# Kernel tuning notes

Measured on AMD Instinct MI355X. Metric: run time of the kernel, lower is better.

The kernel has to match this reference:

```python
import jax, jax.numpy as jnp
import numpy as np

N = 50000   # nodes
D = 128     # hidden dim
E_NS = 250000  # non-self-loop edges
B = 4096    # sessions
NEG_SLOPE = 0.01  # F.leaky_relu default


def setup_inputs() -> dict:
    key = jax.random.key(0)
    ks = jax.random.split(key, 8)
    x = jax.random.normal(ks[0], (N, D), jnp.float32)
    src = jax.random.randint(ks[1], (E_NS,), 0, N)
    off = jax.random.randint(ks[2], (E_NS,), 1, N)
    dst = (src + off) % N  # guarantees src != dst
    loops = jnp.arange(N)
    edge_index = jnp.stack([jnp.concatenate([src, loops]),
                            jnp.concatenate([dst, loops])])  # [2, E_NS+N]
    batch = jnp.sort(jax.random.randint(ks[3], (N,), 0, B))
    local_sess_avg = jax.random.normal(ks[4], (B, D), jnp.float32)
    stdv = 1.0 / np.sqrt(D)
    W_alpha = jax.random.uniform(ks[5], (1, D), jnp.float32, -stdv, stdv)
    W_forward = jax.random.uniform(ks[6], (1, D), jnp.float32, -stdv, stdv)
    W_backward = jax.random.uniform(ks[7], (1, D), jnp.float32, -stdv, stdv)
    mt_sess_masks = jnp.ones((N,), jnp.int32)
    return {"x": x, "W_alpha": W_alpha, "W_forward": W_forward,
            "W_backward": W_backward, "local_sess_avg": local_sess_avg,
            "edge_index": edge_index, "batch": batch,
            "mt_sess_masks": mt_sess_masks, "n_nonself": E_NS}


def reference(x, W_alpha, W_forward, W_backward, local_sess_avg,
              edge_index, batch, mt_sess_masks, n_nonself):
    n = x.shape[0]
    src, dst = edge_index[0], edge_index[1]
    # non-self-loop edges occupy the first n_nonself columns (static int)
    src_ns, dst_ns = src[:n_nonself], dst[:n_nonself]
    # expanded edges = original edges + reversed non-self-loop edges
    exp_src = jnp.concatenate([src, dst_ns])  # [Et]
    exp_dst = jnp.concatenate([dst, src_ns])  # [Et]

    lrelu = lambda v: jax.nn.leaky_relu(v, NEG_SLOPE)

    exp_xi = x[exp_dst]                     # [Et, D]
    exp_xj = x[exp_src]                     # [Et, D]
    alpha_query = local_sess_avg[batch[exp_dst]]  # [Et, D]
    alpha = lrelu((exp_xi * alpha_query) @ W_alpha.T)        # [Et, 1]
    beta = lrelu((x[dst] * x[src]) @ W_forward.T)            # [E, 1]
    rbeta = lrelu((x[dst_ns] * x[src_ns]) @ W_backward.T)    # [E_ns, 1]
    logits = (jnp.concatenate([beta, rbeta], axis=0) + alpha)[:, 0]  # [Et]

    # segment softmax over target nodes (every node has a self-loop)
    seg_max = jax.lax.stop_gradient(
        jax.ops.segment_max(logits, exp_dst, num_segments=n))
    ex = jnp.exp(logits - seg_max[exp_dst])
    denom = jax.ops.segment_sum(ex, exp_dst, num_segments=n)
    aij = ex / denom[exp_dst]

    # scatter-add weighted neighbor features
    aggr = jax.ops.segment_sum(aij[:, None] * exp_xj, exp_dst, num_segments=n)

    # update: masked nodes take aggregate, others keep x; residual add
    new_x = jnp.where((mt_sess_masks == 1)[:, None], aggr, x)
    return new_x + x
```

## Files before the change

kernel.cpp:

```cpp
#include <hip/hip_runtime.h>

#define NEG_SLOPE 0.01f
#define STRIDE 48

__device__ __forceinline__ float lrelu(float v) { return v > 0.f ? v : NEG_SLOPE * v; }

__device__ __forceinline__ float dot4(float4 a, float4 b) {
    return a.x * b.x + a.y * b.y + a.z * b.z + a.w * b.w;
}

__device__ __forceinline__ void placeEdge(int s, int d, unsigned flag,
                                          int* __restrict__ cursor, int* __restrict__ slots) {
    int pos = atomicAdd(&cursor[d], 1);
    if (pos < STRIDE) slots[d * STRIDE + pos] = (int)((unsigned)s | flag);
}

__global__ void fill_kernel(const int* __restrict__ EI0, const int* __restrict__ EI1,
                            int* __restrict__ cursor, int* __restrict__ slots,
                            int E_total, int E_NS) {
    int t = blockIdx.x * blockDim.x + threadIdx.x;
    int n1v = E_total >> 2, n0v = E_NS >> 2;
    if (t < n1v) {
        int4 s = ((const int4*)EI0)[t];
        int4 d = ((const int4*)EI1)[t];
        placeEdge(s.x, d.x, 0u, cursor, slots);
        placeEdge(s.y, d.y, 0u, cursor, slots);
        placeEdge(s.z, d.z, 0u, cursor, slots);
        placeEdge(s.w, d.w, 0u, cursor, slots);
    } else if (t < n1v + n0v) {
        int u = t - n1v;
        int4 s = ((const int4*)EI1)[u];
        int4 d = ((const int4*)EI0)[u];
        placeEdge(s.x, d.x, 0x80000000u, cursor, slots);
        placeEdge(s.y, d.y, 0x80000000u, cursor, slots);
        placeEdge(s.z, d.z, 0x80000000u, cursor, slots);
        placeEdge(s.w, d.w, 0x80000000u, cursor, slots);
    } else if (t == n1v + n0v) {
        for (int e = E_total & ~3; e < E_total; e++)
            placeEdge(EI0[e], EI1[e], 0u, cursor, slots);
        for (int e = E_NS & ~3; e < E_NS; e++)
            placeEdge(EI1[e], EI0[e], 0x80000000u, cursor, slots);
    }
}

__global__ void gather_kernel(const float4* __restrict__ x4,
                              const float4* __restrict__ Wf4, const float4* __restrict__ Wb4,
                              const int* __restrict__ cursor, const int* __restrict__ slots,
                              const int* __restrict__ mask,
                              float4* __restrict__ out4, int N) {
    int tid = blockIdx.x * blockDim.x + threadIdx.x;
    int node = tid >> 4;
    int sub = threadIdx.x & 15;
    bool active = (node < N);
    int nodeSafe = active ? node : 0;

    long long base = (long long)nodeSafe * 32;
    float4 xda = x4[base + sub];
    float4 xdb = x4[base + 16 + sub];
    int msk = active ? mask[nodeSafe] : 0;
    int cnt = (active && msk == 1) ? min(cursor[nodeSafe], STRIDE) : 0;
    const int* myslots = slots + nodeSafe * STRIDE;

    float4 wfa = Wf4[sub], wfb = Wf4[16 + sub];
    float4 wba = Wb4[sub], wbb = Wb4[16 + sub];
    float4 yfa = {xda.x * wfa.x, xda.y * wfa.y, xda.z * wfa.z, xda.w * wfa.w};
    float4 yfb = {xdb.x * wfb.x, xdb.y * wfb.y, xdb.z * wfb.z, xdb.w * wfb.w};
    float4 yba = {xda.x * wba.x, xda.y * wba.y, xda.z * wba.z, xda.w * wba.w};
    float4 ybb = {xdb.x * wbb.x, xdb.y * wbb.y, xdb.z * wbb.z, xdb.w * wbb.w};

    int cm = cnt;
    cm = max(cm, __shfl_xor(cm, 16, 64));
    cm = max(cm, __shfl_xor(cm, 32, 64));

    float l = 0.f;
    float4 Oa = {0.f, 0.f, 0.f, 0.f}, Ob = {0.f, 0.f, 0.f, 0.f};

    for (int i = 0; i < cm; i += 4) {
        int4 ee = *(const int4*)(myslots + i);
        bool v0 = (i < cnt), v1 = (i + 1 < cnt), v2 = (i + 2 < cnt), v3 = (i + 3 < cnt);
        int e0 = v0 ? ee.x : 0, e1 = v1 ? ee.y : 0, e2 = v2 ? ee.z : 0, e3 = v3 ? ee.w : 0;
        long long s0 = (long long)(e0 & 0x7fffffff) * 32;
        long long s1 = (long long)(e1 & 0x7fffffff) * 32;
        long long s2 = (long long)(e2 & 0x7fffffff) * 32;
        long long s3 = (long long)(e3 & 0x7fffffff) * 32;
        float4 r0a = x4[s0 + sub], r0b = x4[s0 + 16 + sub];
        float4 r1a = x4[s1 + sub], r1b = x4[s1 + 16 + sub];
        float4 r2a = x4[s2 + sub], r2b = x4[s2 + 16 + sub];
        float4 r3a = x4[s3 + sub], r3b = x4[s3 + 16 + sub];
        bool f0 = (e0 < 0), f1 = (e1 < 0), f2 = (e2 < 0), f3 = (e3 < 0);

        float p0 = dot4(r0a, f0 ? yba : yfa) + dot4(r0b, f0 ? ybb : yfb);
        float p1 = dot4(r1a, f1 ? yba : yfa) + dot4(r1b, f1 ? ybb : yfb);
        float p2 = dot4(r2a, f2 ? yba : yfa) + dot4(r2b, f2 ? ybb : yfb);
        float p3 = dot4(r3a, f3 ? yba : yfa) + dot4(r3b, f3 ? ybb : yfb);
#pragma unroll
        for (int sh = 1; sh < 16; sh <<= 1) {
            p0 += __shfl_xor(p0, sh, 64);
            p1 += __shfl_xor(p1, sh, 64);
            p2 += __shfl_xor(p2, sh, 64);
            p3 += __shfl_xor(p3, sh, 64);
        }

        float ev0 = v0 ? __expf(lrelu(p0)) : 0.f;
        float ev1 = v1 ? __expf(lrelu(p1)) : 0.f;
        float ev2 = v2 ? __expf(lrelu(p2)) : 0.f;
        float ev3 = v3 ? __expf(lrelu(p3)) : 0.f;
        l += ev0 + ev1 + ev2 + ev3;
        Oa.x += ev0 * r0a.x + ev1 * r1a.x + ev2 * r2a.x + ev3 * r3a.x;
        Oa.y += ev0 * r0a.y + ev1 * r1a.y + ev2 * r2a.y + ev3 * r3a.y;
        Oa.z += ev0 * r0a.z + ev1 * r1a.z + ev2 * r2a.z + ev3 * r3a.z;
        Oa.w += ev0 * r0a.w + ev1 * r1a.w + ev2 * r2a.w + ev3 * r3a.w;
        Ob.x += ev0 * r0b.x + ev1 * r1b.x + ev2 * r2b.x + ev3 * r3b.x;
        Ob.y += ev0 * r0b.y + ev1 * r1b.y + ev2 * r2b.y + ev3 * r3b.y;
        Ob.z += ev0 * r0b.z + ev1 * r1b.z + ev2 * r2b.z + ev3 * r3b.z;
        Ob.w += ev0 * r0b.w + ev1 * r1b.w + ev2 * r2b.w + ev3 * r3b.w;
    }

    if (active) {
        float4 ra, rb;
        if (msk == 1) {
            float inv = (l > 0.f) ? 1.f / l : 0.f;
            ra = {Oa.x * inv + xda.x, Oa.y * inv + xda.y, Oa.z * inv + xda.z, Oa.w * inv + xda.w};
            rb = {Ob.x * inv + xdb.x, Ob.y * inv + xdb.y, Ob.z * inv + xdb.z, Ob.w * inv + xdb.w};
        } else {
            ra = {2.f * xda.x, 2.f * xda.y, 2.f * xda.z, 2.f * xda.w};
            rb = {2.f * xdb.x, 2.f * xdb.y, 2.f * xdb.z, 2.f * xdb.w};
        }
        out4[base + sub] = ra;
        out4[base + 16 + sub] = rb;
    }
}

extern "C" void kernel_launch(void* const* d_in, const int* in_sizes, int n_in,
                              void* d_out, int out_size, void* d_ws, size_t ws_size,
                              hipStream_t stream) {
    const float* x   = (const float*)d_in[0];
    const float* Wf  = (const float*)d_in[2];
    const float* Wb  = (const float*)d_in[3];
    const int* EI    = (const int*)d_in[5];
    const int* mask  = (const int*)d_in[7];

    int N = in_sizes[6];
    int E_total = in_sizes[5] / 2;
    int E_NS = E_total - N;

    const int* EI0 = EI;
    const int* EI1 = EI + E_total;

    char* ws = (char*)d_ws;
    int* cursor = (int*)ws;
    int* slots  = (int*)(ws + (size_t)N * 4);

    hipMemsetAsync(cursor, 0, (size_t)N * 4, stream);

    const int BLK = 256;
    int edgeVecThreads = (E_total >> 2) + (E_NS >> 2) + 1;
    int edgeVecBlocks = (edgeVecThreads + BLK - 1) / BLK;
    int nodeBlocks = ((N * 16) + BLK - 1) / BLK;

    fill_kernel<<<edgeVecBlocks, BLK, 0, stream>>>(EI0, EI1, cursor, slots, E_total, E_NS);
    gather_kernel<<<nodeBlocks, BLK, 0, stream>>>(
        (const float4*)x, (const float4*)Wf, (const float4*)Wb,
        cursor, slots, mask, (float4*)d_out, N);
}
```

Baseline: 157.4 us.

## Gather neighbor features from a bf16 copy of x built in the fill kernel

Adds a conversion pass, fused into the edge-fill kernel, that writes a bf16 copy of x to workspace. The gather kernel then reads neighbor rows as bf16 (uint4 of 8 values per lane), halving the bytes moved by the random gathers. Lanes now own 8 contiguous features, and both forward and backward dot products are computed so the direction select happens on the scalar. The cost is an extra full read/write pass over x plus bf16 rounding error in the attention logits and the aggregated features.

```diff
diff --git a/kernel.cpp b/kernel.cpp
--- a/kernel.cpp
+++ b/kernel.cpp
@@ -5,9 +5,15 @@
 
 __device__ __forceinline__ float lrelu(float v) { return v > 0.f ? v : NEG_SLOPE * v; }
 
-__device__ __forceinline__ float dot4(float4 a, float4 b) {
-    return a.x * b.x + a.y * b.y + a.z * b.z + a.w * b.w;
+__device__ __forceinline__ unsigned pack_bf16(float a, float b) {
+    unsigned ua = __float_as_uint(a);
+    ua = (ua + 0x7fffu + ((ua >> 16) & 1u)) >> 16;
+    unsigned ub = __float_as_uint(b);
+    ub = (ub + 0x7fffu + ((ub >> 16) & 1u)) & 0xffff0000u;
+    return ua | ub;
 }
+__device__ __forceinline__ float blo(unsigned u) { return __uint_as_float(u << 16); }
+__device__ __forceinline__ float bhi(unsigned u) { return __uint_as_float(u & 0xffff0000u); }
 
 __device__ __forceinline__ void placeEdge(int s, int d, unsigned flag,
                                           int* __restrict__ cursor, int* __restrict__ slots) {
@@ -15,27 +21,39 @@
     if (pos < STRIDE) slots[d * STRIDE + pos] = (int)((unsigned)s | flag);
 }
 
-__global__ void fill_kernel(const int* __restrict__ EI0, const int* __restrict__ EI1,
+__global__ void prep_kernel(const float4* __restrict__ x4, uint4* __restrict__ xh,
+                            const int* __restrict__ EI0, const int* __restrict__ EI1,
                             int* __restrict__ cursor, int* __restrict__ slots,
-                            int E_total, int E_NS) {
+                            int E_total, int E_NS, int nConvert) {
     int t = blockIdx.x * blockDim.x + threadIdx.x;
+    if (t < nConvert) {
+        float4 a = x4[2 * t], b = x4[2 * t + 1];
+        uint4 o;
+        o.x = pack_bf16(a.x, a.y);
+        o.y = pack_bf16(a.z, a.w);
+        o.z = pack_bf16(b.x, b.y);
+        o.w = pack_bf16(b.z, b.w);
+        xh[t] = o;
+        return;
+    }
+    int u = t - nConvert;
     int n1v = E_total >> 2, n0v = E_NS >> 2;
-    if (t < n1v) {
-        int4 s = ((const int4*)EI0)[t];
-        int4 d = ((const int4*)EI1)[t];
+    if (u < n1v) {
+        int4 s = ((const int4*)EI0)[u];
+        int4 d = ((const int4*)EI1)[u];
         placeEdge(s.x, d.x, 0u, cursor, slots);
         placeEdge(s.y, d.y, 0u, cursor, slots);
         placeEdge(s.z, d.z, 0u, cursor, slots);
         placeEdge(s.w, d.w, 0u, cursor, slots);
-    } else if (t < n1v + n0v) {
-        int u = t - n1v;
-        int4 s = ((const int4*)EI1)[u];
-        int4 d = ((const int4*)EI0)[u];
+    } else if (u < n1v + n0v) {
+        int v = u - n1v;
+        int4 s = ((const int4*)EI1)[v];
+        int4 d = ((const int4*)EI0)[v];
         placeEdge(s.x, d.x, 0x80000000u, cursor, slots);
         placeEdge(s.y, d.y, 0x80000000u, cursor, slots);
         placeEdge(s.z, d.z, 0x80000000u, cursor, slots);
         placeEdge(s.w, d.w, 0x80000000u, cursor, slots);
-    } else if (t == n1v + n0v) {
+    } else if (u == n1v + n0v) {
         for (int e = E_total & ~3; e < E_total; e++)
             placeEdge(EI0[e], EI1[e], 0u, cursor, slots);
         for (int e = E_NS & ~3; e < E_NS; e++)
@@ -43,7 +61,12 @@
     }
 }
 
-__global__ void gather_kernel(const float4* __restrict__ x4,
+__device__ __forceinline__ float dot8u(uint4 h, float4 y0, float4 y1) {
+    return blo(h.x) * y0.x + bhi(h.x) * y0.y + blo(h.y) * y0.z + bhi(h.y) * y0.w +
+           blo(h.z) * y1.x + bhi(h.z) * y1.y + blo(h.w) * y1.z + bhi(h.w) * y1.w;
+}
+
+__global__ void gather_kernel(const float4* __restrict__ x4, const uint4* __restrict__ xh,
                               const float4* __restrict__ Wf4, const float4* __restrict__ Wb4,
                               const int* __restrict__ cursor, const int* __restrict__ slots,
                               const int* __restrict__ mask,
@@ -55,44 +78,44 @@
     int nodeSafe = active ? node : 0;
 
     long long base = (long long)nodeSafe * 32;
-    float4 xda = x4[base + sub];
-    float4 xdb = x4[base + 16 + sub];
+    float4 xd0 = x4[base + 2 * sub];
+    float4 xd1 = x4[base + 2 * sub + 1];
     int msk = active ? mask[nodeSafe] : 0;
     int cnt = (active && msk == 1) ? min(cursor[nodeSafe], STRIDE) : 0;
     const int* myslots = slots + nodeSafe * STRIDE;
 
-    float4 wfa = Wf4[sub], wfb = Wf4[16 + sub];
-    float4 wba = Wb4[sub], wbb = Wb4[16 + sub];
-    float4 yfa = {xda.x * wfa.x, xda.y * wfa.y, xda.z * wfa.z, xda.w * wfa.w};
-    float4 yfb = {xdb.x * wfb.x, xdb.y * wfb.y, xdb.z * wfb.z, xdb.w * wfb.w};
-    float4 yba = {xda.x * wba.x, xda.y * wba.y, xda.z * wba.z, xda.w * wba.w};
-    float4 ybb = {xdb.x * wbb.x, xdb.y * wbb.y, xdb.z * wbb.z, xdb.w * wbb.w};
+    float4 wf0 = Wf4[2 * sub], wf1 = Wf4[2 * sub + 1];
+    float4 wb0 = Wb4[2 * sub], wb1 = Wb4[2 * sub + 1];
+    float4 yf0 = {xd0.x * wf0.x, xd0.y * wf0.y, xd0.z * wf0.z, xd0.w * wf0.w};
+    float4 yf1 = {xd1.x * wf1.x, xd1.y * wf1.y, xd1.z * wf1.z, xd1.w * wf1.w};
+    float4 yb0 = {xd0.x * wb0.x, xd0.y * wb0.y, xd0.z * wb0.z, xd0.w * wb0.w};
+    float4 yb1 = {xd1.x * wb1.x, xd1.y * wb1.y, xd1.z * wb1.z, xd1.w * wb1.w};
 
     int cm = cnt;
     cm = max(cm, __shfl_xor(cm, 16, 64));
     cm = max(cm, __shfl_xor(cm, 32, 64));
 
     float l = 0.f;
-    float4 Oa = {0.f, 0.f, 0.f, 0.f}, Ob = {0.f, 0.f, 0.f, 0.f};
+    float4 O0 = {0.f, 0.f, 0.f, 0.f}, O1 = {0.f, 0.f, 0.f, 0.f};
 
     for (int i = 0; i < cm; i += 4) {
         int4 ee = *(const int4*)(myslots + i);
         bool v0 = (i < cnt), v1 = (i + 1 < cnt), v2 = (i + 2 < cnt), v3 = (i + 3 < cnt);
         int e0 = v0 ? ee.x : 0, e1 = v1 ? ee.y : 0, e2 = v2 ? ee.z : 0, e3 = v3 ? ee.w : 0;
-        long long s0 = (long long)(e0 & 0x7fffffff) * 32;
-        long long s1 = (long long)(e1 & 0x7fffffff) * 32;
-        long long s2 = (long long)(e2 & 0x7fffffff) * 32;
-        long long s3 = (long long)(e3 & 0x7fffffff) * 32;
-        float4 r0a = x4[s0 + sub], r0b = x4[s0 + 16 + sub];
-        float4 r1a = x4[s1 + sub], r1b = x4[s1 + 16 + sub];
-        float4 r2a = x4[s2 + sub], r2b = x4[s2 + 16 + sub];
-        float4 r3a = x4[s3 + sub], r3b = x4[s3 + 16 + sub];
-        bool f0 = (e0 < 0), f1 = (e1 < 0), f2 = (e2 < 0), f3 = (e3 < 0);
+        uint4 h0 = xh[(long long)(e0 & 0x7fffffff) * 16 + sub];
+        uint4 h1 = xh[(long long)(e1 & 0x7fffffff) * 16 + sub];
+        uint4 h2 = xh[(long long)(e2 & 0x7fffffff) * 16 + sub];
+        uint4 h3 = xh[(long long)(e3 & 0x7fffffff) * 16 + sub];
 
-        float p0 = dot4(r0a, f0 ? yba : yfa) + dot4(r0b, f0 ? ybb : yfb);
-        float p1 = dot4(r1a, f1 ? yba : yfa) + dot4(r1b, f1 ? ybb : yfb);
-        float p2 = dot4(r2a, f2 ? yba : yfa) + dot4(r2b, f2 ? ybb : yfb);
-        float p3 = dot4(r3a, f3 ? yba : yfa) + dot4(r3b, f3 ? ybb : yfb);
+        float pf0 = dot8u(h0, yf0, yf1), pb0 = dot8u(h0, yb0, yb1);
+        float pf1 = dot8u(h1, yf0, yf1), pb1 = dot8u(h1, yb0, yb1);
+        float pf2 = dot8u(h2, yf0, yf1), pb2 = dot8u(h2, yb0, yb1);
+        float pf3 = dot8u(h3, yf0, yf1), pb3 = dot8u(h3, yb0, yb1);
+        float p0 = (e0 < 0) ? pb0 : pf0;
+        float p1 = (e1 < 0) ? pb1 : pf1;
+        float p2 = (e2 < 0) ? pb2 : pf2;
+        float p3 = (e3 < 0) ? pb3 : pf3;
+
 #pragma unroll
         for (int sh = 1; sh < 16; sh <<= 1) {
             p0 += __shfl_xor(p0, sh, 64);
@@ -106,28 +129,29 @@
         float ev2 = v2 ? __expf(lrelu(p2)) : 0.f;
         float ev3 = v3 ? __expf(lrelu(p3)) : 0.f;
         l += ev0 + ev1 + ev2 + ev3;
-        Oa.x += ev0 * r0a.x + ev1 * r1a.x + ev2 * r2a.x + ev3 * r3a.x;
-        Oa.y += ev0 * r0a.y + ev1 * r1a.y + ev2 * r2a.y + ev3 * r3a.y;
-        Oa.z += ev0 * r0a.z + ev1 * r1a.z + ev2 * r2a.z + ev3 * r3a.z;
-        Oa.w += ev0 * r0a.w + ev1 * r1a.w + ev2 * r2a.w + ev3 * r3a.w;
-        Ob.x += ev0 * r0b.x + ev1 * r1b.x + ev2 * r2b.x + ev3 * r3b.x;
-        Ob.y += ev0 * r0b.y + ev1 * r1b.y + ev2 * r2b.y + ev3 * r3b.y;
-        Ob.z += ev0 * r0b.z + ev1 * r1b.z + ev2 * r2b.z + ev3 * r3b.z;
-        Ob.w += ev0 * r0b.w + ev1 * r1b.w + ev2 * r2b.w + ev3 * r3b.w;
+
+        O0.x += ev0 * blo(h0.x) + ev1 * blo(h1.x) + ev2 * blo(h2.x) + ev3 * blo(h3.x);
+        O0.y += ev0 * bhi(h0.x) + ev1 * bhi(h1.x) + ev2 * bhi(h2.x) + ev3 * bhi(h3.x);
+        O0.z += ev0 * blo(h0.y) + ev1 * blo(h1.y) + ev2 * blo(h2.y) + ev3 * blo(h3.y);
+        O0.w += ev0 * bhi(h0.y) + ev1 * bhi(h1.y) + ev2 * bhi(h2.y) + ev3 * bhi(h3.y);
+        O1.x += ev0 * blo(h0.z) + ev1 * blo(h1.z) + ev2 * blo(h2.z) + ev3 * blo(h3.z);
+        O1.y += ev0 * bhi(h0.z) + ev1 * bhi(h1.z) + ev2 * bhi(h2.z) + ev3 * bhi(h3.z);
+        O1.z += ev0 * blo(h0.w) + ev1 * blo(h1.w) + ev2 * blo(h2.w) + ev3 * blo(h3.w);
+        O1.w += ev0 * bhi(h0.w) + ev1 * bhi(h1.w) + ev2 * bhi(h2.w) + ev3 * bhi(h3.w);
     }
 
     if (active) {
         float4 ra, rb;
         if (msk == 1) {
             float inv = (l > 0.f) ? 1.f / l : 0.f;
-            ra = {Oa.x * inv + xda.x, Oa.y * inv + xda.y, Oa.z * inv + xda.z, Oa.w * inv + xda.w};
-            rb = {Ob.x * inv + xdb.x, Ob.y * inv + xdb.y, Ob.z * inv + xdb.z, Ob.w * inv + xdb.w};
+            ra = {O0.x * inv + xd0.x, O0.y * inv + xd0.y, O0.z * inv + xd0.z, O0.w * inv + xd0.w};
+            rb = {O1.x * inv + xd1.x, O1.y * inv + xd1.y, O1.z * inv + xd1.z, O1.w * inv + xd1.w};
         } else {
-            ra = {2.f * xda.x, 2.f * xda.y, 2.f * xda.z, 2.f * xda.w};
-            rb = {2.f * xdb.x, 2.f * xdb.y, 2.f * xdb.z, 2.f * xdb.w};
+            ra = {2.f * xd0.x, 2.f * xd0.y, 2.f * xd0.z, 2.f * xd0.w};
+            rb = {2.f * xd1.x, 2.f * xd1.y, 2.f * xd1.z, 2.f * xd1.w};
         }
-        out4[base + sub] = ra;
-        out4[base + 16 + sub] = rb;
+        out4[base + 2 * sub] = ra;
+        out4[base + 2 * sub + 1] = rb;
     }
 }
 
@@ -150,16 +174,19 @@
     char* ws = (char*)d_ws;
     int* cursor = (int*)ws;
     int* slots  = (int*)(ws + (size_t)N * 4);
+    uint4* xh   = (uint4*)(ws + (size_t)N * 4 * (1 + STRIDE));
 
     hipMemsetAsync(cursor, 0, (size_t)N * 4, stream);
 
     const int BLK = 256;
-    int edgeVecThreads = (E_total >> 2) + (E_NS >> 2) + 1;
-    int edgeVecBlocks = (edgeVecThreads + BLK - 1) / BLK;
+    int nConvert = N * 16;
+    int fillThreads = (E_total >> 2) + (E_NS >> 2) + 1;
+    int prepBlocks = (nConvert + fillThreads + BLK - 1) / BLK;
     int nodeBlocks = ((N * 16) + BLK - 1) / BLK;
 
-    fill_kernel<<<edgeVecBlocks, BLK, 0, stream>>>(EI0, EI1, cursor, slots, E_total, E_NS);
+    prep_kernel<<<prepBlocks, BLK, 0, stream>>>((const float4*)x, xh, EI0, EI1,
+                                                cursor, slots, E_total, E_NS, nConvert);
     gather_kernel<<<nodeBlocks, BLK, 0, stream>>>(
-        (const float4*)x, (const float4*)Wf, (const float4*)Wb,
+        (const float4*)x, (const uint4*)xh, (const float4*)Wf, (const float4*)Wb,
         cursor, slots, mask, (float4*)d_out, N);
 }
```

Result: no change. 160.2 us (+1.8%).
